# Optimization experiments

Hardware: AMD Instinct MI355X
Metric: run time of the kernel (lower is better)

The kernel has to match this reference:

```python
import jax, jax.numpy as jnp
import numpy as np

N_NODES = 4096
EMB_DIM = 512
N_HEADS = 8
K_SPARSE = 128
HEAD_DIM = EMB_DIM // N_HEADS


def setup_inputs() -> dict:
    key = jax.random.key(0)
    k1, k2, k3, k4 = jax.random.split(key, 4)
    # xavier_uniform bound for square [D, D] weight
    bound = float(np.sqrt(6.0 / (EMB_DIM + EMB_DIM)))
    return {
        "embedding_matrix": jax.random.normal(k1, (N_NODES, EMB_DIM), dtype=jnp.float32),
        "Wq": jax.random.uniform(k2, (EMB_DIM, EMB_DIM), minval=-bound, maxval=bound, dtype=jnp.float32),
        "bq": jnp.zeros((EMB_DIM,), dtype=jnp.float32),
        "Wk": jax.random.uniform(k3, (EMB_DIM, EMB_DIM), minval=-bound, maxval=bound, dtype=jnp.float32),
        "bk": jnp.zeros((EMB_DIM,), dtype=jnp.float32),
        "sparse_indices": jax.random.randint(k4, (N_HEADS, N_NODES, K_SPARSE), 0, N_NODES, dtype=jnp.int32),
    }


def reference(embedding_matrix, Wq, bq, Wk, bk, sparse_indices):
    N, D = embedding_matrix.shape
    H, _, K = sparse_indices.shape
    hd = D // H
    # torch Linear: y = x @ W.T + b
    q = (embedding_matrix @ Wq.T + bq).reshape(N, H, hd).transpose(1, 0, 2)  # [H, N, hd]
    kk = (embedding_matrix @ Wk.T + bk).reshape(N, H, hd).transpose(1, 0, 2)  # [H, N, hd]
    # per-head gather of K random keys per query node: [H, N, K, hd]
    sel = jax.vmap(lambda kh, ih: kh[ih])(kk, sparse_indices)
    scores = jnp.einsum("hnd,hnkd->hnk", q, sel) / jnp.sqrt(jnp.float32(hd))  # [H, N, K]
    h_idx = jnp.arange(H)[:, None, None]
    n_idx = jnp.arange(N)[None, :, None]
    out = jnp.zeros((H, N, N), dtype=scores.dtype).at[h_idx, n_idx, sparse_indices].set(scores)
    return out
```

## Files before the change

kernel.cpp:

```cpp
#include <hip/hip_runtime.h>
#include <hip/hip_bf16.h>
#include <stdint.h>

#define N_NODES  4096
#define EMB_DIM  512
#define N_HEADS  8
#define K_SPARSE 128
#define HEAD_DIM 64

typedef __attribute__((ext_vector_type(8))) __bf16 bf16x8;
typedef __attribute__((ext_vector_type(4))) float  f32x4;

__device__ __forceinline__ float bf2f(unsigned short u) {
    union { unsigned int i; float f; } v;
    v.i = ((unsigned int)u) << 16;
    return v.f;
}

__device__ __forceinline__ unsigned short f2bf(float f) {
    union { float f; unsigned int i; } v;
    v.f = f;
    unsigned int x = v.i;
    unsigned int rounding = 0x7fffu + ((x >> 16) & 1u);
    x += rounding;
    return (unsigned short)(x >> 16);
}

__global__ __launch_bounds__(256) void proj_kernel(
    const float* __restrict__ X,
    const float* __restrict__ Wq, const float* __restrict__ bq,
    const float* __restrict__ Wk, const float* __restrict__ bk,
    unsigned short* __restrict__ Qb, unsigned short* __restrict__ Kb)
{
    __shared__ unsigned short As[64][40];
    __shared__ unsigned short Bs[128][40];

    const float* __restrict__ W    = blockIdx.z ? Wk : Wq;
    const float* __restrict__ bias = blockIdx.z ? bk : bq;
    unsigned short* __restrict__ out = blockIdx.z ? Kb : Qb;

    const int t    = threadIdx.x;
    const int M0   = blockIdx.x * 64;
    const int N0   = blockIdx.y * 128;
    const int lane = t & 63;
    const int wave = t >> 6;
    const int wm   = (wave >> 1) * 32;
    const int wn   = (wave & 1) * 64;

    const int arow = t >> 2;
    const int acol = (t & 3) * 8;
    const int brow = t >> 1;
    const int bcol = (t & 1) * 16;

    f32x4 acc[2][4] = {};

    for (int kt = 0; kt < EMB_DIM / 32; ++kt) {
        const int k0 = kt * 32;
        {
            const float4* srcA = (const float4*)(X + (size_t)(M0 + arow) * EMB_DIM + k0 + acol);
            float4 va0 = srcA[0], va1 = srcA[1];
            unsigned int pa[4];
            pa[0] = (unsigned int)f2bf(va0.x) | ((unsigned int)f2bf(va0.y) << 16);
            pa[1] = (unsigned int)f2bf(va0.z) | ((unsigned int)f2bf(va0.w) << 16);
            pa[2] = (unsigned int)f2bf(va1.x) | ((unsigned int)f2bf(va1.y) << 16);
            pa[3] = (unsigned int)f2bf(va1.z) | ((unsigned int)f2bf(va1.w) << 16);
            *(uint4*)&As[arow][acol] = make_uint4(pa[0], pa[1], pa[2], pa[3]);

            const float4* srcB = (const float4*)(W + (size_t)(N0 + brow) * EMB_DIM + k0 + bcol);
            unsigned int pb[8];
            #pragma unroll
            for (int c = 0; c < 4; ++c) {
                float4 vb = srcB[c];
                pb[c * 2 + 0] = (unsigned int)f2bf(vb.x) | ((unsigned int)f2bf(vb.y) << 16);
                pb[c * 2 + 1] = (unsigned int)f2bf(vb.z) | ((unsigned int)f2bf(vb.w) << 16);
            }
            uint4* dstB = (uint4*)&Bs[brow][bcol];
            dstB[0] = make_uint4(pb[0], pb[1], pb[2], pb[3]);
            dstB[1] = make_uint4(pb[4], pb[5], pb[6], pb[7]);
        }
        __syncthreads();

        bf16x8 af[2], bff[4];
        #pragma unroll
        for (int i = 0; i < 2; ++i)
            af[i] = __builtin_bit_cast(bf16x8,
                *(const uint4*)&As[wm + i * 16 + (lane & 15)][(lane >> 4) * 8]);
        #pragma unroll
        for (int i = 0; i < 4; ++i)
            bff[i] = __builtin_bit_cast(bf16x8,
                *(const uint4*)&Bs[wn + i * 16 + (lane & 15)][(lane >> 4) * 8]);

        #pragma unroll
        for (int mi = 0; mi < 2; ++mi)
            #pragma unroll
            for (int ni = 0; ni < 4; ++ni)
                acc[mi][ni] = __builtin_amdgcn_mfma_f32_16x16x32_bf16(
                    af[mi], bff[ni], acc[mi][ni], 0, 0, 0);
        __syncthreads();
    }

    #pragma unroll
    for (int mi = 0; mi < 2; ++mi) {
        #pragma unroll
        for (int ni = 0; ni < 4; ++ni) {
            const int col = N0 + wn + ni * 16 + (lane & 15);
            const float bval = bias[col];
            #pragma unroll
            for (int r = 0; r < 4; ++r) {
                const int row = M0 + wm + mi * 16 + (lane >> 4) * 4 + r;
                out[(size_t)row * EMB_DIM + col] = f2bf(acc[mi][ni][r] + bval);
            }
        }
    }
}

__global__ __launch_bounds__(256) void scatter_kernel(
    const unsigned short* __restrict__ Qb,
    const unsigned short* __restrict__ Kb,
    const int* __restrict__ sidx,
    float* __restrict__ out)
{
    __shared__ float rowbuf[N_NODES];
    __shared__ int   sIdx[K_SPARSE];

    const int t = threadIdx.x;
    const int b = blockIdx.x;
    const int h = b >> 12;
    const int n = b & (N_NODES - 1);
    const int j = t & 7;

    const uint4 qu = *(const uint4*)(Qb + (size_t)n * EMB_DIM + h * HEAD_DIM + j * 8);
    int myIdxLd = 0;
    if (t < K_SPARSE)
        myIdxLd = sidx[((size_t)(h * N_NODES + n)) * K_SPARSE + t];

    f32x4* rowv = (f32x4*)rowbuf;
    const f32x4 z4 = {0.0f, 0.0f, 0.0f, 0.0f};
    #pragma unroll
    for (int i = 0; i < 4; ++i) rowv[t + 256 * i] = z4;

    if (t < K_SPARSE) sIdx[t] = myIdxLd;

    float q[8];
    {
        unsigned int uu[4] = {qu.x, qu.y, qu.z, qu.w};
        #pragma unroll
        for (int w = 0; w < 4; ++w) {
            q[2 * w + 0] = bf2f((unsigned short)(uu[w] & 0xffffu));
            q[2 * w + 1] = bf2f((unsigned short)(uu[w] >> 16));
        }
    }
    __syncthreads();

    unsigned int* tags = (unsigned int*)rowbuf;
    if (t < K_SPARSE) atomicMax(&tags[myIdxLd], (unsigned int)(t + 1));

    float score[4];
    int   kidx[4];
    #pragma unroll
    for (int iter = 0; iter < 4; ++iter) {
        const int kk  = (t >> 3) + 32 * iter;
        const int idx = sIdx[kk];
        kidx[iter] = idx;
        const uint4 u = *(const uint4*)(Kb + (size_t)idx * EMB_DIM + h * HEAD_DIM + j * 8);
        unsigned int uu[4] = {u.x, u.y, u.z, u.w};
        float acc = 0.0f;
        #pragma unroll
        for (int w = 0; w < 4; ++w) {
            acc += bf2f((unsigned short)(uu[w] & 0xffffu)) * q[2 * w + 0];
            acc += bf2f((unsigned short)(uu[w] >> 16))     * q[2 * w + 1];
        }
        acc += __shfl_xor(acc, 1);
        acc += __shfl_xor(acc, 2);
        acc += __shfl_xor(acc, 4);
        score[iter] = acc * 0.125f;
    }

    __syncthreads();

    bool win[4];
    #pragma unroll
    for (int iter = 0; iter < 4; ++iter) {
        const int kk = (t >> 3) + 32 * iter;
        win[iter] = (j == 0) && (tags[kidx[iter]] == (unsigned int)(kk + 1));
    }

    __syncthreads();

    #pragma unroll
    for (int iter = 0; iter < 4; ++iter)
        if (win[iter]) rowbuf[kidx[iter]] = score[iter];

    __syncthreads();

    f32x4* orowv = (f32x4*)(out + ((size_t)(h * N_NODES + n)) * N_NODES);
    #pragma unroll
    for (int i = 0; i < 4; ++i)
        __builtin_nontemporal_store(rowv[t + 256 * i], &orowv[t + 256 * i]);
}

extern "C" void kernel_launch(void* const* d_in, const int* in_sizes, int n_in,
                              void* d_out, int out_size, void* d_ws, size_t ws_size,
                              hipStream_t stream) {
    const float* emb = (const float*)d_in[0];
    const float* Wq  = (const float*)d_in[1];
    const float* bq  = (const float*)d_in[2];
    const float* Wk  = (const float*)d_in[3];
    const float* bk  = (const float*)d_in[4];
    const int*   si  = (const int*)d_in[5];
    float* out = (float*)d_out;

    unsigned short* Qb = (unsigned short*)d_ws;
    unsigned short* Kb = Qb + (size_t)N_NODES * EMB_DIM;

    dim3 pg(N_NODES / 64, EMB_DIM / 128, 2);
    proj_kernel<<<pg, 256, 0, stream>>>(emb, Wq, bq, Wk, bk, Qb, Kb);

    scatter_kernel<<<N_HEADS * N_NODES, 256, 0, stream>>>(Qb, Kb, si, out);
}
```

Baseline: 558.9 us.

## Split gather-score and dense row expansion into separate kernels

The fused score-and-scatter kernel is split into a score kernel, which writes compact per-row scores to a workspace buffer, and an expand kernel, which zero-fills each dense row in shared memory, resolves duplicate indices with atomicMax, and streams the row out. The intent is to separate the latency-bound gather phase from the bandwidth-bound 512 MB output write so that each kernel runs at better occupancy and the write stream is not stalled by gathers. In exchange it adds a kernel launch, a workspace round trip for scores and indices, and a second read of the index array.

```diff
diff --git a/kernel.cpp b/kernel.cpp
--- a/kernel.cpp
+++ b/kernel.cpp
@@ -114,14 +114,14 @@
     }
 }
 
-__global__ __launch_bounds__(256) void scatter_kernel(
+__global__ __launch_bounds__(256) void score_kernel(
     const unsigned short* __restrict__ Qb,
     const unsigned short* __restrict__ Kb,
     const int* __restrict__ sidx,
-    float* __restrict__ out)
+    float* __restrict__ scores)
 {
-    __shared__ float rowbuf[N_NODES];
     __shared__ int   sIdx[K_SPARSE];
+    __shared__ float sSc[K_SPARSE];
 
     const int t = threadIdx.x;
     const int b = blockIdx.x;
@@ -130,16 +130,8 @@
     const int j = t & 7;
 
     const uint4 qu = *(const uint4*)(Qb + (size_t)n * EMB_DIM + h * HEAD_DIM + j * 8);
-    int myIdxLd = 0;
     if (t < K_SPARSE)
-        myIdxLd = sidx[((size_t)(h * N_NODES + n)) * K_SPARSE + t];
-
-    f32x4* rowv = (f32x4*)rowbuf;
-    const f32x4 z4 = {0.0f, 0.0f, 0.0f, 0.0f};
-    #pragma unroll
-    for (int i = 0; i < 4; ++i) rowv[t + 256 * i] = z4;
-
-    if (t < K_SPARSE) sIdx[t] = myIdxLd;
+        sIdx[t] = sidx[((size_t)b) * K_SPARSE + t];
 
     float q[8];
     {
@@ -152,16 +144,10 @@
     }
     __syncthreads();
 
-    unsigned int* tags = (unsigned int*)rowbuf;
-    if (t < K_SPARSE) atomicMax(&tags[myIdxLd], (unsigned int)(t + 1));
-
-    float score[4];
-    int   kidx[4];
     #pragma unroll
     for (int iter = 0; iter < 4; ++iter) {
         const int kk  = (t >> 3) + 32 * iter;
         const int idx = sIdx[kk];
-        kidx[iter] = idx;
         const uint4 u = *(const uint4*)(Kb + (size_t)idx * EMB_DIM + h * HEAD_DIM + j * 8);
         unsigned int uu[4] = {u.x, u.y, u.z, u.w};
         float acc = 0.0f;
@@ -173,27 +159,48 @@
         acc += __shfl_xor(acc, 1);
         acc += __shfl_xor(acc, 2);
         acc += __shfl_xor(acc, 4);
-        score[iter] = acc * 0.125f;
-    }
-
-    __syncthreads();
-
-    bool win[4];
-    #pragma unroll
-    for (int iter = 0; iter < 4; ++iter) {
-        const int kk = (t >> 3) + 32 * iter;
-        win[iter] = (j == 0) && (tags[kidx[iter]] == (unsigned int)(kk + 1));
-    }
-
-    __syncthreads();
-
-    #pragma unroll
-    for (int iter = 0; iter < 4; ++iter)
-        if (win[iter]) rowbuf[kidx[iter]] = score[iter];
-
-    __syncthreads();
-
-    f32x4* orowv = (f32x4*)(out + ((size_t)(h * N_NODES + n)) * N_NODES);
+        if (j == 0) sSc[kk] = acc * 0.125f;
+    }
+    __syncthreads();
+
+    if (t < K_SPARSE)
+        scores[(size_t)b * K_SPARSE + t] = sSc[t];
+}
+
+__global__ __launch_bounds__(256) void expand_kernel(
+    const int* __restrict__ sidx,
+    const float* __restrict__ scores,
+    float* __restrict__ out)
+{
+    __shared__ float rowbuf[N_NODES];
+
+    const int t = threadIdx.x;
+    const int b = blockIdx.x;
+
+    int   idx = 0;
+    float sc  = 0.0f;
+    if (t < K_SPARSE) {
+        idx = sidx[(size_t)b * K_SPARSE + t];
+        sc  = scores[(size_t)b * K_SPARSE + t];
+    }
+
+    f32x4* rowv = (f32x4*)rowbuf;
+    const f32x4 z4 = {0.0f, 0.0f, 0.0f, 0.0f};
+    #pragma unroll
+    for (int i = 0; i < 4; ++i) rowv[t + 256 * i] = z4;
+    __syncthreads();
+
+    unsigned int* tags = (unsigned int*)rowbuf;
+    if (t < K_SPARSE) atomicMax(&tags[idx], (unsigned int)(t + 1));
+    __syncthreads();
+
+    const bool win = (t < K_SPARSE) && (tags[idx] == (unsigned int)(t + 1));
+    __syncthreads();
+
+    if (win) rowbuf[idx] = sc;
+    __syncthreads();
+
+    f32x4* orowv = (f32x4*)(out + (size_t)b * N_NODES);
     #pragma unroll
     for (int i = 0; i < 4; ++i)
         __builtin_nontemporal_store(rowv[t + 256 * i], &orowv[t + 256 * i]);
@@ -212,9 +219,12 @@
 
     unsigned short* Qb = (unsigned short*)d_ws;
     unsigned short* Kb = Qb + (size_t)N_NODES * EMB_DIM;
+    float* scoresBuf   = (float*)(Kb + (size_t)N_NODES * EMB_DIM);
 
     dim3 pg(N_NODES / 64, EMB_DIM / 128, 2);
     proj_kernel<<<pg, 256, 0, stream>>>(emb, Wq, bq, Wk, bk, Qb, Kb);
 
-    scatter_kernel<<<N_HEADS * N_NODES, 256, 0, stream>>>(Qb, Kb, si, out);
-}
+    score_kernel<<<N_HEADS * N_NODES, 256, 0, stream>>>(Qb, Kb, si, scoresBuf);
+
+    expand_kernel<<<N_HEADS * N_NODES, 256, 0, stream>>>(si, scoresBuf, out);
+}
```

New measurement: 607.4 us. +8.7%, slower.

## Shrink scatter kernel to single-wave blocks and replace barriers with waitcnt

Applied to the files above, without the earlier changes.

The scatter kernel now uses 64-thread blocks, so one wavefront handles a whole output row. Indices stay in registers and are shared with __shfl instead of going through LDS, and the __syncthreads barriers become s_waitcnt lgkmcnt(0), which relies on ordering inside one wave. Each thread now does 16 key gathers and 16 row stores instead of 4. LDS use per block is still 16KB, so occupancy may be limited by LDS rather than by thread count. Correctness depends on LDS operations within a single wave completing in order.

```diff
diff --git a/kernel.cpp b/kernel.cpp
--- a/kernel.cpp
+++ b/kernel.cpp
@@ -114,32 +114,29 @@
     }
 }
 
-__global__ __launch_bounds__(256) void scatter_kernel(
+__global__ __launch_bounds__(64) void scatter_kernel(
     const unsigned short* __restrict__ Qb,
     const unsigned short* __restrict__ Kb,
     const int* __restrict__ sidx,
     float* __restrict__ out)
 {
     __shared__ float rowbuf[N_NODES];
-    __shared__ int   sIdx[K_SPARSE];
 
     const int t = threadIdx.x;
     const int b = blockIdx.x;
     const int h = b >> 12;
     const int n = b & (N_NODES - 1);
     const int j = t & 7;
-
+    const int g = t >> 3;
+
+    const int myIdx0 = sidx[(size_t)b * K_SPARSE + t];
+    const int myIdx1 = sidx[(size_t)b * K_SPARSE + 64 + t];
     const uint4 qu = *(const uint4*)(Qb + (size_t)n * EMB_DIM + h * HEAD_DIM + j * 8);
-    int myIdxLd = 0;
-    if (t < K_SPARSE)
-        myIdxLd = sidx[((size_t)(h * N_NODES + n)) * K_SPARSE + t];
 
     f32x4* rowv = (f32x4*)rowbuf;
     const f32x4 z4 = {0.0f, 0.0f, 0.0f, 0.0f};
     #pragma unroll
-    for (int i = 0; i < 4; ++i) rowv[t + 256 * i] = z4;
-
-    if (t < K_SPARSE) sIdx[t] = myIdxLd;
+    for (int i = 0; i < 16; ++i) rowv[t + 64 * i] = z4;
 
     float q[8];
     {
@@ -150,18 +147,19 @@
             q[2 * w + 1] = bf2f((unsigned short)(uu[w] >> 16));
         }
     }
-    __syncthreads();
 
     unsigned int* tags = (unsigned int*)rowbuf;
-    if (t < K_SPARSE) atomicMax(&tags[myIdxLd], (unsigned int)(t + 1));
-
-    float score[4];
-    int   kidx[4];
-    #pragma unroll
-    for (int iter = 0; iter < 4; ++iter) {
-        const int kk  = (t >> 3) + 32 * iter;
-        const int idx = sIdx[kk];
-        kidx[iter] = idx;
+    asm volatile("s_waitcnt lgkmcnt(0)" ::: "memory");
+    atomicMax(&tags[myIdx0], (unsigned int)(t + 1));
+    atomicMax(&tags[myIdx1], (unsigned int)(t + 65));
+
+    float score[16];
+    int   kidx[16];
+    #pragma unroll
+    for (int p = 0; p < 16; ++p) {
+        const int kk  = g + 8 * p;
+        const int idx = (p < 8) ? __shfl(myIdx0, kk) : __shfl(myIdx1, kk - 64);
+        kidx[p] = idx;
         const uint4 u = *(const uint4*)(Kb + (size_t)idx * EMB_DIM + h * HEAD_DIM + j * 8);
         unsigned int uu[4] = {u.x, u.y, u.z, u.w};
         float acc = 0.0f;
@@ -173,30 +171,28 @@
         acc += __shfl_xor(acc, 1);
         acc += __shfl_xor(acc, 2);
         acc += __shfl_xor(acc, 4);
-        score[iter] = acc * 0.125f;
-    }
-
-    __syncthreads();
-
-    bool win[4];
-    #pragma unroll
-    for (int iter = 0; iter < 4; ++iter) {
-        const int kk = (t >> 3) + 32 * iter;
-        win[iter] = (j == 0) && (tags[kidx[iter]] == (unsigned int)(kk + 1));
-    }
-
-    __syncthreads();
-
-    #pragma unroll
-    for (int iter = 0; iter < 4; ++iter)
-        if (win[iter]) rowbuf[kidx[iter]] = score[iter];
-
-    __syncthreads();
-
-    f32x4* orowv = (f32x4*)(out + ((size_t)(h * N_NODES + n)) * N_NODES);
-    #pragma unroll
-    for (int i = 0; i < 4; ++i)
-        __builtin_nontemporal_store(rowv[t + 256 * i], &orowv[t + 256 * i]);
+        score[p] = acc * 0.125f;
+    }
+
+    asm volatile("s_waitcnt lgkmcnt(0)" ::: "memory");
+    if (j == 0) {
+        unsigned int winmask = 0;
+        #pragma unroll
+        for (int p = 0; p < 16; ++p)
+            if (tags[kidx[p]] == (unsigned int)(g + 8 * p + 1)) winmask |= (1u << p);
+        asm volatile("s_waitcnt lgkmcnt(0)" ::: "memory");
+        #pragma unroll
+        for (int p = 0; p < 16; ++p)
+            if (winmask & (1u << p)) rowbuf[kidx[p]] = score[p];
+    }
+    asm volatile("s_waitcnt lgkmcnt(0)" ::: "memory");
+
+    f32x4* orowv = (f32x4*)(out + (size_t)b * N_NODES);
+    #pragma unroll
+    for (int i = 0; i < 16; ++i) {
+        f32x4 v = rowv[t + 64 * i];
+        __builtin_nontemporal_store(v, &orowv[t + 64 * i]);
+    }
 }
 
 extern "C" void kernel_launch(void* const* d_in, const int* in_sizes, int n_in,
@@ -216,5 +212,5 @@
     dim3 pg(N_NODES / 64, EMB_DIM / 128, 2);
     proj_kernel<<<pg, 256, 0, stream>>>(emb, Wq, bq, Wk, bk, Qb, Kb);
 
-    scatter_kernel<<<N_HEADS * N_NODES, 256, 0, stream>>>(Qb, Kb, si, out);
-}
+    scatter_kernel<<<N_HEADS * N_NODES, 64, 0, stream>>>(Qb, Kb, si, out);
+}
```

Result: slower. 579.6 us (+3.7%).
